# Kernel optimization log

Hardware: AMD Instinct MI355X
Metric: run time of the kernel (lower is better)

## Reference

```python
import jax, jax.numpy as jnp
import numpy as np
import math

HIDDEN = 1024
HEADS = 16
HEAD_DIM = HIDDEN // HEADS
TEMP_K = 1000.0  # custom temperature multiplier applied after masking
B, S = 2, 2048


def setup_inputs() -> dict:
    key = jax.random.key(0)
    ks = jax.random.split(key, 4)
    scale = 1.0 / math.sqrt(HIDDEN)
    return {
        "x": jax.random.normal(ks[0], (B, S, HIDDEN), dtype=jnp.float32),
        "W_qkv": jax.random.normal(ks[1], (HIDDEN, 3 * HIDDEN), dtype=jnp.float32) * scale,
        "b_qkv": jnp.zeros((3 * HIDDEN,), dtype=jnp.float32),
        "W_out": jax.random.normal(ks[2], (HIDDEN, HIDDEN), dtype=jnp.float32) * scale,
        "b_out": jnp.zeros((HIDDEN,), dtype=jnp.float32),
    }


def reference(x, W_qkv, b_qkv, W_out, b_out):
    b, s, _ = x.shape
    qkv = x @ W_qkv + b_qkv                                    # [b,s,3*hidden]
    qkv = qkv.reshape(b, s, 3, HEADS, HEAD_DIM)
    qkv = jnp.transpose(qkv, (2, 0, 3, 1, 4))                  # [3,b,h,s,d]
    q, k, v = qkv[0], qkv[1], qkv[2]
    scores = jnp.einsum('bhqd,bhkd->bhqk', q, k) / math.sqrt(HEAD_DIM)
    causal = jnp.tril(jnp.ones((s, s), dtype=bool))            # [s,s]
    scores = jnp.where(causal[None, None], scores, -jnp.inf)
    probs = jax.nn.softmax(scores * TEMP_K, axis=-1)           # temp-scaled softmax
    attn = jnp.einsum('bhqk,bhkd->bhqd', probs, v)             # [b,h,s,d]
    attn = jnp.transpose(attn, (0, 2, 1, 3)).reshape(b, s, HIDDEN)
    return attn @ W_out + b_out
```

## Files before the change

### kernel.cpp

```cpp
#include <hip/hip_runtime.h>
#include <hip/hip_bf16.h>

#define BATCH 2
#define SEQ 2048
#define HID 1024
#define NHEAD 16
#define HDIM 64
#define LSCALE 125.0f
#define NEGBIG (-1.0e30f)

typedef __bf16 bf16;
typedef __bf16 bf16x4 __attribute__((ext_vector_type(4)));
typedef __bf16 bf16x8 __attribute__((ext_vector_type(8)));
typedef float f32x16 __attribute__((ext_vector_type(16)));

__global__ __launch_bounds__(256) void transpose_split_kernel(
    const float* __restrict__ W, bf16* __restrict__ Thi, bf16* __restrict__ Tlo,
    int K, int N)
{
    __shared__ float T[64][65];
    const int tid = threadIdx.x;
    const int kBase = blockIdx.y * 64;
    const int nBase = blockIdx.x * 64;
    {
        const int k0 = tid >> 4;
        const int nc = (tid & 15) * 4;
#pragma unroll
        for (int kk = 0; kk < 4; kk++) {
            int k = k0 + kk * 16;
            float4 v = *(const float4*)(W + (size_t)(kBase + k) * N + nBase + nc);
            T[k][nc] = v.x; T[k][nc + 1] = v.y; T[k][nc + 2] = v.z; T[k][nc + 3] = v.w;
        }
    }
    __syncthreads();
    {
        const int n = tid >> 2;
        const int kc = (tid & 3) * 16;
        bf16x8 h0, h1, l0, l1;
#pragma unroll
        for (int j = 0; j < 8; j++) {
            float a = T[kc + j][n];
            float c = T[kc + 8 + j][n];
            bf16 ha = (bf16)a, hc = (bf16)c;
            h0[j] = ha; h1[j] = hc;
            l0[j] = (bf16)(a - (float)ha);
            l1[j] = (bf16)(c - (float)hc);
        }
        size_t dst = (size_t)(nBase + n) * K + kBase + kc;
        *(bf16x8*)(Thi + dst)     = h0;
        *(bf16x8*)(Thi + dst + 8) = h1;
        if (Tlo) {
            *(bf16x8*)(Tlo + dst)     = l0;
            *(bf16x8*)(Tlo + dst + 8) = l1;
        }
    }
}

__global__ __launch_bounds__(256) void gemm_qkv_mfma(
    const float* __restrict__ X, const bf16* __restrict__ Wthi,
    const bf16* __restrict__ Wtlo, const float* __restrict__ bias,
    bf16* __restrict__ qhi, bf16* __restrict__ qlo,
    bf16* __restrict__ khi, bf16* __restrict__ klo, bf16* __restrict__ vv)
{
    __shared__ __align__(16) bf16 Xh[128][40];
    __shared__ __align__(16) bf16 Xl[128][40];
    __shared__ __align__(16) bf16 Wh[128][40];
    __shared__ __align__(16) bf16 Wl[128][40];

    const int tid = threadIdx.x;
    const int wave = tid >> 6, lane = tid & 63;
    const int lm = lane & 31, lq2 = lane >> 5;
    const int wave_s = wave & 1, wave_n = wave >> 1;
    const int nBase = blockIdx.x * 128;
    const int sBase = blockIdx.y * 128;
    const bool isV = (nBase >= 2 * HID);

    const int sr = tid >> 1, skc = (tid & 1) * 16;

    f32x16 acc[2][2];
#pragma unroll
    for (int st = 0; st < 2; st++)
#pragma unroll
      for (int nt = 0; nt < 2; nt++)
#pragma unroll
        for (int r = 0; r < 16; r++) acc[st][nt][r] = 0.f;

    for (int k0 = 0; k0 < HID; k0 += 32) {
        const float4* px = (const float4*)(X + (size_t)(sBase + sr) * HID + k0 + skc);
        float4 x0 = px[0], x1 = px[1], x2 = px[2], x3 = px[3];
        size_t wsrc = (size_t)(nBase + sr) * HID + k0 + skc;
        bf16x8 wh0 = *(const bf16x8*)(Wthi + wsrc);
        bf16x8 wh1 = *(const bf16x8*)(Wthi + wsrc + 8);
        bf16x8 wl0 = {}, wl1 = {};
        if (!isV) {
            wl0 = *(const bf16x8*)(Wtlo + wsrc);
            wl1 = *(const bf16x8*)(Wtlo + wsrc + 8);
        }
        __syncthreads();
        {
            float xs[16] = {x0.x, x0.y, x0.z, x0.w, x1.x, x1.y, x1.z, x1.w,
                            x2.x, x2.y, x2.z, x2.w, x3.x, x3.y, x3.z, x3.w};
            bf16x8 hh0, hh1;
#pragma unroll
            for (int j = 0; j < 8; j++) { hh0[j] = (bf16)xs[j]; hh1[j] = (bf16)xs[j + 8]; }
            *(bf16x8*)&Xh[sr][skc]     = hh0;
            *(bf16x8*)&Xh[sr][skc + 8] = hh1;
            if (!isV) {
                bf16x8 ll0, ll1;
#pragma unroll
                for (int j = 0; j < 8; j++) {
                    ll0[j] = (bf16)(xs[j] - (float)hh0[j]);
                    ll1[j] = (bf16)(xs[j + 8] - (float)hh1[j]);
                }
                *(bf16x8*)&Xl[sr][skc]     = ll0;
                *(bf16x8*)&Xl[sr][skc + 8] = ll1;
            }
        }
        *(bf16x8*)&Wh[sr][skc]     = wh0;
        *(bf16x8*)&Wh[sr][skc + 8] = wh1;
        if (!isV) {
            *(bf16x8*)&Wl[sr][skc]     = wl0;
            *(bf16x8*)&Wl[sr][skc + 8] = wl1;
        }
        __syncthreads();

#pragma unroll
        for (int kh = 0; kh < 2; kh++) {
            const int ko = kh * 16 + lq2 * 8;
            bf16x8 aWh[2], aWl[2], bXh[2], bXl[2];
#pragma unroll
            for (int nt = 0; nt < 2; nt++) {
                aWh[nt] = *(bf16x8*)&Wh[wave_n * 64 + nt * 32 + lm][ko];
                if (!isV) aWl[nt] = *(bf16x8*)&Wl[wave_n * 64 + nt * 32 + lm][ko];
            }
#pragma unroll
            for (int st = 0; st < 2; st++) {
                bXh[st] = *(bf16x8*)&Xh[wave_s * 64 + st * 32 + lm][ko];
                if (!isV) bXl[st] = *(bf16x8*)&Xl[wave_s * 64 + st * 32 + lm][ko];
            }
#pragma unroll
            for (int nt = 0; nt < 2; nt++)
#pragma unroll
              for (int st = 0; st < 2; st++) {
                acc[st][nt] = __builtin_amdgcn_mfma_f32_32x32x16_bf16(aWh[nt], bXh[st], acc[st][nt], 0, 0, 0);
                if (!isV) {
                    acc[st][nt] = __builtin_amdgcn_mfma_f32_32x32x16_bf16(aWh[nt], bXl[st], acc[st][nt], 0, 0, 0);
                    acc[st][nt] = __builtin_amdgcn_mfma_f32_32x32x16_bf16(aWl[nt], bXh[st], acc[st][nt], 0, 0, 0);
                }
              }
        }
    }

#pragma unroll
    for (int st = 0; st < 2; st++) {
        int s = sBase + wave_s * 64 + st * 32 + lm;
        int bb = s >> 11, ss = s & 2047;
#pragma unroll
        for (int nt = 0; nt < 2; nt++) {
#pragma unroll
            for (int q4 = 0; q4 < 4; q4++) {
                int n = nBase + wave_n * 64 + nt * 32 + 8 * q4 + 4 * lq2;
                float4 bv = *(const float4*)(bias + n);
                float vals[4];
                vals[0] = acc[st][nt][q4 * 4 + 0] + bv.x;
                vals[1] = acc[st][nt][q4 * 4 + 1] + bv.y;
                vals[2] = acc[st][nt][q4 * 4 + 2] + bv.z;
                vals[3] = acc[st][nt][q4 * 4 + 3] + bv.w;
                int which = n >> 10, h = (n >> 6) & 15, d = n & 63;
                size_t dst = (((size_t)bb * NHEAD + h) * SEQ + ss) * HDIM + d;
                if (which < 2) {
                    bf16x4 hi4, lo4;
#pragma unroll
                    for (int i = 0; i < 4; i++) {
                        hi4[i] = (bf16)vals[i];
                        lo4[i] = (bf16)(vals[i] - (float)hi4[i]);
                    }
                    bf16* ph = (which == 0) ? qhi : khi;
                    bf16* pl = (which == 0) ? qlo : klo;
                    *(bf16x4*)(ph + dst) = hi4;
                    *(bf16x4*)(pl + dst) = lo4;
                } else {
                    bf16x4 v4;
#pragma unroll
                    for (int i = 0; i < 4; i++) v4[i] = (bf16)vals[i];
                    *(bf16x4*)(vv + dst) = v4;
                }
            }
        }
    }
}

__global__ __launch_bounds__(256) void attn_kernel(
    const bf16* __restrict__ Qhi, const bf16* __restrict__ Qlo,
    const bf16* __restrict__ Khg, const bf16* __restrict__ Klg,
    const bf16* __restrict__ Vg, bf16* __restrict__ attnbuf)
{
    __shared__ __align__(16) bf16 Khs[64][72];
    __shared__ __align__(16) bf16 Kls[64][72];
    __shared__ __align__(16) bf16 Vt [64][72];
    __shared__ __align__(16) bf16 Pb [128][72];

    const int tid  = threadIdx.x;
    const int wave = tid >> 6;
    const int lane = tid & 63;
    const int lm   = lane & 31;
    const int lq2  = lane >> 5;

    const int qt = 15 - blockIdx.x;
    const int bh = blockIdx.y;
    const int b = bh >> 4, h = bh & 15;
    const size_t headoff = ((size_t)b * NHEAD + h) * SEQ * HDIM;

    const int qg = qt * 128 + wave * 32 + lm;
    bf16x8 qh[4], ql[4];
    {
        const bf16* qph = Qhi + headoff + (size_t)qg * HDIM;
        const bf16* qpl = Qlo + headoff + (size_t)qg * HDIM;
#pragma unroll
        for (int c = 0; c < 4; c++) {
            qh[c] = *(const bf16x8*)(qph + c * 16 + lq2 * 8);
            ql[c] = *(const bf16x8*)(qpl + c * 16 + lq2 * 8);
        }
    }

    const int kr  = tid >> 2;
    const int kd0 = (tid & 3) * 16;
    const int vd  = tid & 63;
    const int vc0 = (tid >> 6) * 16;

    f32x16 O0, O1;
#pragma unroll
    for (int r = 0; r < 16; r++) { O0[r] = 0.f; O1[r] = 0.f; }
    float m_run = NEGBIG, l_run = 0.f;

    const int ktmax = 2 * qt + 1;
    for (int kt = 0; kt <= ktmax; kt++) {
        size_t kbase_g = headoff + (size_t)(kt * 64 + kr) * HDIM + kd0;
        bf16x8 kh0 = *(const bf16x8*)(Khg + kbase_g);
        bf16x8 kh1 = *(const bf16x8*)(Khg + kbase_g + 8);
        bf16x8 kl0 = *(const bf16x8*)(Klg + kbase_g);
        bf16x8 kl1 = *(const bf16x8*)(Klg + kbase_g + 8);
        bf16 vtmp[16];
#pragma unroll
        for (int i = 0; i < 16; i++)
            vtmp[i] = Vg[headoff + (size_t)(kt * 64 + vc0 + i) * HDIM + vd];

        __syncthreads();

        *(bf16x8*)&Khs[kr][kd0]     = kh0;
        *(bf16x8*)&Khs[kr][kd0 + 8] = kh1;
        *(bf16x8*)&Kls[kr][kd0]     = kl0;
        *(bf16x8*)&Kls[kr][kd0 + 8] = kl1;
        {
            bf16x8 v0, v1;
#pragma unroll
            for (int i = 0; i < 8; i++) { v0[i] = vtmp[i]; v1[i] = vtmp[i + 8]; }
            *(bf16x8*)&Vt[vd][vc0]     = v0;
            *(bf16x8*)&Vt[vd][vc0 + 8] = v1;
        }
        __syncthreads();

        f32x16 s0, s1;
#pragma unroll
        for (int r = 0; r < 16; r++) { s0[r] = 0.f; s1[r] = 0.f; }
#pragma unroll
        for (int c = 0; c < 4; c++) {
            bf16x8 ah0 = *(bf16x8*)&Khs[lm][c * 16 + lq2 * 8];
            bf16x8 al0 = *(bf16x8*)&Kls[lm][c * 16 + lq2 * 8];
            bf16x8 ah1 = *(bf16x8*)&Khs[32 + lm][c * 16 + lq2 * 8];
            bf16x8 al1 = *(bf16x8*)&Kls[32 + lm][c * 16 + lq2 * 8];
            s0 = __builtin_amdgcn_mfma_f32_32x32x16_bf16(ah0, qh[c], s0, 0, 0, 0);
            s0 = __builtin_amdgcn_mfma_f32_32x32x16_bf16(ah0, ql[c], s0, 0, 0, 0);
            s0 = __builtin_amdgcn_mfma_f32_32x32x16_bf16(al0, qh[c], s0, 0, 0, 0);
            s1 = __builtin_amdgcn_mfma_f32_32x32x16_bf16(ah1, qh[c], s1, 0, 0, 0);
            s1 = __builtin_amdgcn_mfma_f32_32x32x16_bf16(ah1, ql[c], s1, 0, 0, 0);
            s1 = __builtin_amdgcn_mfma_f32_32x32x16_bf16(al1, qh[c], s1, 0, 0, 0);
        }

        float logit[2][16];
        const int kbase = kt * 64 + 4 * lq2;
        const bool needmask = (kt * 64 + 63 > qg);
#pragma unroll
        for (int r = 0; r < 16; r++) {
            int koff = (r & 3) + 8 * (r >> 2);
            float L0 = s0[r] * LSCALE;
            float L1 = s1[r] * LSCALE;
            if (needmask) {
                if (kbase + koff > qg) L0 = NEGBIG;
                if (kbase + 32 + koff > qg) L1 = NEGBIG;
            }
            logit[0][r] = L0;
            logit[1][r] = L1;
        }

        float vmax = NEGBIG;
#pragma unroll
        for (int r = 0; r < 16; r++)
            vmax = fmaxf(vmax, fmaxf(logit[0][r], logit[1][r]));
        vmax = fmaxf(vmax, __shfl_xor(vmax, 32, 64));
        float mnew = fmaxf(m_run, vmax);
        float alpha = __expf(m_run - mnew);
        float p[2][16];
        float sum = 0.f;
#pragma unroll
        for (int r = 0; r < 16; r++) {
            p[0][r] = __expf(logit[0][r] - mnew);
            p[1][r] = __expf(logit[1][r] - mnew);
            sum += p[0][r] + p[1][r];
        }
        sum += __shfl_xor(sum, 32, 64);
        l_run = l_run * alpha + sum;
        m_run = mnew;
#pragma unroll
        for (int r = 0; r < 16; r++) { O0[r] *= alpha; O1[r] *= alpha; }

#pragma unroll
        for (int mt = 0; mt < 2; mt++)
#pragma unroll
          for (int g = 0; g < 4; g++) {
            bf16x4 pk;
            pk[0] = (bf16)p[mt][4 * g + 0];
            pk[1] = (bf16)p[mt][4 * g + 1];
            pk[2] = (bf16)p[mt][4 * g + 2];
            pk[3] = (bf16)p[mt][4 * g + 3];
            *(bf16x4*)&Pb[wave * 32 + lm][mt * 32 + 8 * g + 4 * lq2] = pk;
          }
        asm volatile("s_waitcnt lgkmcnt(0)" ::: "memory");

#pragma unroll
        for (int c = 0; c < 4; c++) {
            bf16x8 pb  = *(bf16x8*)&Pb[wave * 32 + lm][c * 16 + lq2 * 8];
            bf16x8 va0 = *(bf16x8*)&Vt[lm][c * 16 + lq2 * 8];
            bf16x8 va1 = *(bf16x8*)&Vt[32 + lm][c * 16 + lq2 * 8];
            O0 = __builtin_amdgcn_mfma_f32_32x32x16_bf16(va0, pb, O0, 0, 0, 0);
            O1 = __builtin_amdgcn_mfma_f32_32x32x16_bf16(va1, pb, O1, 0, 0, 0);
        }
    }

    const float inv = 1.0f / l_run;
    bf16* orow = attnbuf + ((size_t)b * SEQ + qg) * HID + h * HDIM;
#pragma unroll
    for (int g = 0; g < 4; g++) {
        int d0 = 8 * g + 4 * lq2;
        bf16x4 o0, o1;
#pragma unroll
        for (int i = 0; i < 4; i++) {
            o0[i] = (bf16)(O0[4 * g + i] * inv);
            o1[i] = (bf16)(O1[4 * g + i] * inv);
        }
        *(bf16x4*)(orow + d0)      = o0;
        *(bf16x4*)(orow + 32 + d0) = o1;
    }
}

__global__ __launch_bounds__(256) void gemm_out_mfma(
    const bf16* __restrict__ Attn, const bf16* __restrict__ Wt,
    const float* __restrict__ bias, float* __restrict__ out)
{
    __shared__ __align__(16) bf16 Ah[128][40];
    __shared__ __align__(16) bf16 Bh[128][40];

    const int tid = threadIdx.x;
    const int wave = tid >> 6, lane = tid & 63;
    const int lm = lane & 31, lq2 = lane >> 5;
    const int wave_m = wave & 1, wave_n = wave >> 1;
    const int nBase = blockIdx.x * 128;
    const int mBase = blockIdx.y * 128;

    const int sr = tid >> 1, skc = (tid & 1) * 16;

    f32x16 acc[2][2];
#pragma unroll
    for (int mt = 0; mt < 2; mt++)
#pragma unroll
      for (int nt = 0; nt < 2; nt++)
#pragma unroll
        for (int r = 0; r < 16; r++) acc[mt][nt][r] = 0.f;

    for (int k0 = 0; k0 < HID; k0 += 32) {
        size_t asrc = (size_t)(nBase + sr) * HID + k0 + skc;
        size_t bsrc = (size_t)(mBase + sr) * HID + k0 + skc;
        bf16x8 a0 = *(const bf16x8*)(Wt + asrc);
        bf16x8 a1 = *(const bf16x8*)(Wt + asrc + 8);
        bf16x8 b0 = *(const bf16x8*)(Attn + bsrc);
        bf16x8 b1 = *(const bf16x8*)(Attn + bsrc + 8);
        __syncthreads();
        *(bf16x8*)&Ah[sr][skc]     = a0;
        *(bf16x8*)&Ah[sr][skc + 8] = a1;
        *(bf16x8*)&Bh[sr][skc]     = b0;
        *(bf16x8*)&Bh[sr][skc + 8] = b1;
        __syncthreads();
#pragma unroll
        for (int kh = 0; kh < 2; kh++) {
            const int ko = kh * 16 + lq2 * 8;
            bf16x8 aW[2], bA[2];
#pragma unroll
            for (int nt = 0; nt < 2; nt++)
                aW[nt] = *(bf16x8*)&Ah[wave_n * 64 + nt * 32 + lm][ko];
#pragma unroll
            for (int mt = 0; mt < 2; mt++)
                bA[mt] = *(bf16x8*)&Bh[wave_m * 64 + mt * 32 + lm][ko];
#pragma unroll
            for (int nt = 0; nt < 2; nt++)
#pragma unroll
              for (int mt = 0; mt < 2; mt++)
                acc[mt][nt] = __builtin_amdgcn_mfma_f32_32x32x16_bf16(aW[nt], bA[mt], acc[mt][nt], 0, 0, 0);
        }
    }

#pragma unroll
    for (int mt = 0; mt < 2; mt++) {
        int m = mBase + wave_m * 64 + mt * 32 + lm;
#pragma unroll
        for (int nt = 0; nt < 2; nt++) {
#pragma unroll
            for (int q4 = 0; q4 < 4; q4++) {
                int n = nBase + wave_n * 64 + nt * 32 + 8 * q4 + 4 * lq2;
                float4 bv = *(const float4*)(bias + n);
                float4 o;
                o.x = acc[mt][nt][q4 * 4 + 0] + bv.x;
                o.y = acc[mt][nt][q4 * 4 + 1] + bv.y;
                o.z = acc[mt][nt][q4 * 4 + 2] + bv.z;
                o.w = acc[mt][nt][q4 * 4 + 3] + bv.w;
                *(float4*)(out + (size_t)m * HID + n) = o;
            }
        }
    }
}

extern "C" void kernel_launch(void* const* d_in, const int* in_sizes, int n_in,
                              void* d_out, int out_size, void* d_ws, size_t ws_size,
                              hipStream_t stream) {
    const float* x    = (const float*)d_in[0];
    const float* Wqkv = (const float*)d_in[1];
    const float* bqkv = (const float*)d_in[2];
    const float* Wout = (const float*)d_in[3];
    const float* bout = (const float*)d_in[4];
    float* out = (float*)d_out;

    const size_t NW  = (size_t)HID * 3 * HID;
    const size_t NWo = (size_t)HID * HID;
    const size_t NT  = (size_t)BATCH * NHEAD * SEQ * HDIM;
    bf16* Wthi = (bf16*)d_ws;
    bf16* Wtlo = Wthi + NW;
    bf16* Wot  = Wtlo + NW;
    bf16* qhi  = Wot + NWo;
    bf16* qlo  = qhi + NT;
    bf16* khi  = qlo + NT;
    bf16* klo  = khi + NT;
    bf16* vv   = klo + NT;
    bf16* attnbuf = vv + NT;

    transpose_split_kernel<<<dim3(3 * HID / 64, HID / 64), 256, 0, stream>>>(
        Wqkv, Wthi, Wtlo, HID, 3 * HID);
    transpose_split_kernel<<<dim3(HID / 64, HID / 64), 256, 0, stream>>>(
        Wout, Wot, nullptr, HID, HID);
    gemm_qkv_mfma<<<dim3(3 * HID / 128, BATCH * SEQ / 128), 256, 0, stream>>>(
        x, Wthi, Wtlo, bqkv, qhi, qlo, khi, klo, vv);
    attn_kernel<<<dim3(SEQ / 128, BATCH * NHEAD), 256, 0, stream>>>(
        qhi, qlo, khi, klo, vv, attnbuf);
    gemm_out_mfma<<<dim3(HID / 128, BATCH * SEQ / 128), 256, 0, stream>>>(
        attnbuf, Wot, bout, out);
}
```

Measured before the change: 289.2 us.

## Pre-split X, add atomic work queue to attention, shrink output GEMM tile

A new kernel converts X into bf16 hi/lo halves once, so the QKV GEMM stops redoing that conversion in every N-block and reads half as many bytes per element. The attention kernel becomes persistent: 768 blocks pull (query-tile, head) items from an atomic counter, heaviest causal tiles first, to balance the uneven causal work across CUs. The output GEMM uses 128x64 tiles instead of 128x128, doubling the block count to fill the GPU better. The costs are an extra launch plus hi/lo X buffers that reuse the attention output workspace, atomic contention on one counter, and less data reuse per block in the output GEMM.

After: 298.7 us. 1.03x slower.

```diff
diff --git a/kernel.cpp b/kernel.cpp
--- a/kernel.cpp
+++ b/kernel.cpp
@@ -8,6 +8,7 @@
 #define HDIM 64
 #define LSCALE 125.0f
 #define NEGBIG (-1.0e30f)
+#define N_ITEMS 512
 
 typedef __bf16 bf16;
 typedef __bf16 bf16x4 __attribute__((ext_vector_type(4)));
@@ -56,9 +57,28 @@
     }
 }
 
+__global__ __launch_bounds__(256) void xsplit_kernel(
+    const float* __restrict__ X, bf16* __restrict__ Xhi, bf16* __restrict__ Xlo,
+    unsigned* __restrict__ ctr)
+{
+    if (blockIdx.x == 0 && threadIdx.x == 0) *ctr = 0u;
+    const int i = blockIdx.x * 256 + threadIdx.x;
+    float4 v = ((const float4*)X)[i];
+    float xs[4] = {v.x, v.y, v.z, v.w};
+    bf16x4 h, l;
+#pragma unroll
+    for (int j = 0; j < 4; j++) {
+        h[j] = (bf16)xs[j];
+        l[j] = (bf16)(xs[j] - (float)h[j]);
+    }
+    ((bf16x4*)Xhi)[i] = h;
+    ((bf16x4*)Xlo)[i] = l;
+}
+
 __global__ __launch_bounds__(256) void gemm_qkv_mfma(
-    const float* __restrict__ X, const bf16* __restrict__ Wthi,
-    const bf16* __restrict__ Wtlo, const float* __restrict__ bias,
+    const bf16* __restrict__ Xhi, const bf16* __restrict__ Xlo,
+    const bf16* __restrict__ Wthi, const bf16* __restrict__ Wtlo,
+    const float* __restrict__ bias,
     bf16* __restrict__ qhi, bf16* __restrict__ qlo,
     bf16* __restrict__ khi, bf16* __restrict__ klo, bf16* __restrict__ vv)
 {
@@ -86,39 +106,27 @@
         for (int r = 0; r < 16; r++) acc[st][nt][r] = 0.f;
 
     for (int k0 = 0; k0 < HID; k0 += 32) {
-        const float4* px = (const float4*)(X + (size_t)(sBase + sr) * HID + k0 + skc);
-        float4 x0 = px[0], x1 = px[1], x2 = px[2], x3 = px[3];
+        size_t xsrc = (size_t)(sBase + sr) * HID + k0 + skc;
         size_t wsrc = (size_t)(nBase + sr) * HID + k0 + skc;
+        bf16x8 xh0 = *(const bf16x8*)(Xhi + xsrc);
+        bf16x8 xh1 = *(const bf16x8*)(Xhi + xsrc + 8);
         bf16x8 wh0 = *(const bf16x8*)(Wthi + wsrc);
         bf16x8 wh1 = *(const bf16x8*)(Wthi + wsrc + 8);
-        bf16x8 wl0 = {}, wl1 = {};
+        bf16x8 xl0 = {}, xl1 = {}, wl0 = {}, wl1 = {};
         if (!isV) {
+            xl0 = *(const bf16x8*)(Xlo + xsrc);
+            xl1 = *(const bf16x8*)(Xlo + xsrc + 8);
             wl0 = *(const bf16x8*)(Wtlo + wsrc);
             wl1 = *(const bf16x8*)(Wtlo + wsrc + 8);
         }
         __syncthreads();
-        {
-            float xs[16] = {x0.x, x0.y, x0.z, x0.w, x1.x, x1.y, x1.z, x1.w,
-                            x2.x, x2.y, x2.z, x2.w, x3.x, x3.y, x3.z, x3.w};
-            bf16x8 hh0, hh1;
-#pragma unroll
-            for (int j = 0; j < 8; j++) { hh0[j] = (bf16)xs[j]; hh1[j] = (bf16)xs[j + 8]; }
-            *(bf16x8*)&Xh[sr][skc]     = hh0;
-            *(bf16x8*)&Xh[sr][skc + 8] = hh1;
-            if (!isV) {
-                bf16x8 ll0, ll1;
-#pragma unroll
-                for (int j = 0; j < 8; j++) {
-                    ll0[j] = (bf16)(xs[j] - (float)hh0[j]);
-                    ll1[j] = (bf16)(xs[j + 8] - (float)hh1[j]);
-                }
-                *(bf16x8*)&Xl[sr][skc]     = ll0;
-                *(bf16x8*)&Xl[sr][skc + 8] = ll1;
-            }
-        }
+        *(bf16x8*)&Xh[sr][skc]     = xh0;
+        *(bf16x8*)&Xh[sr][skc + 8] = xh1;
         *(bf16x8*)&Wh[sr][skc]     = wh0;
         *(bf16x8*)&Wh[sr][skc + 8] = wh1;
         if (!isV) {
+            *(bf16x8*)&Xl[sr][skc]     = xl0;
+            *(bf16x8*)&Xl[sr][skc + 8] = xl1;
             *(bf16x8*)&Wl[sr][skc]     = wl0;
             *(bf16x8*)&Wl[sr][skc + 8] = wl1;
         }
@@ -193,12 +201,14 @@
 __global__ __launch_bounds__(256) void attn_kernel(
     const bf16* __restrict__ Qhi, const bf16* __restrict__ Qlo,
     const bf16* __restrict__ Khg, const bf16* __restrict__ Klg,
-    const bf16* __restrict__ Vg, bf16* __restrict__ attnbuf)
+    const bf16* __restrict__ Vg, bf16* __restrict__ attnbuf,
+    unsigned* __restrict__ ctr)
 {
     __shared__ __align__(16) bf16 Khs[64][72];
     __shared__ __align__(16) bf16 Kls[64][72];
     __shared__ __align__(16) bf16 Vt [64][72];
     __shared__ __align__(16) bf16 Pb [128][72];
+    __shared__ int s_item;
 
     const int tid  = threadIdx.x;
     const int wave = tid >> 6;
@@ -206,150 +216,156 @@
     const int lm   = lane & 31;
     const int lq2  = lane >> 5;
 
-    const int qt = 15 - blockIdx.x;
-    const int bh = blockIdx.y;
-    const int b = bh >> 4, h = bh & 15;
-    const size_t headoff = ((size_t)b * NHEAD + h) * SEQ * HDIM;
-
-    const int qg = qt * 128 + wave * 32 + lm;
-    bf16x8 qh[4], ql[4];
-    {
-        const bf16* qph = Qhi + headoff + (size_t)qg * HDIM;
-        const bf16* qpl = Qlo + headoff + (size_t)qg * HDIM;
-#pragma unroll
-        for (int c = 0; c < 4; c++) {
-            qh[c] = *(const bf16x8*)(qph + c * 16 + lq2 * 8);
-            ql[c] = *(const bf16x8*)(qpl + c * 16 + lq2 * 8);
-        }
-    }
-
     const int kr  = tid >> 2;
     const int kd0 = (tid & 3) * 16;
     const int vd  = tid & 63;
     const int vc0 = (tid >> 6) * 16;
 
-    f32x16 O0, O1;
-#pragma unroll
-    for (int r = 0; r < 16; r++) { O0[r] = 0.f; O1[r] = 0.f; }
-    float m_run = NEGBIG, l_run = 0.f;
-
-    const int ktmax = 2 * qt + 1;
-    for (int kt = 0; kt <= ktmax; kt++) {
-        size_t kbase_g = headoff + (size_t)(kt * 64 + kr) * HDIM + kd0;
-        bf16x8 kh0 = *(const bf16x8*)(Khg + kbase_g);
-        bf16x8 kh1 = *(const bf16x8*)(Khg + kbase_g + 8);
-        bf16x8 kl0 = *(const bf16x8*)(Klg + kbase_g);
-        bf16x8 kl1 = *(const bf16x8*)(Klg + kbase_g + 8);
-        bf16 vtmp[16];
-#pragma unroll
-        for (int i = 0; i < 16; i++)
-            vtmp[i] = Vg[headoff + (size_t)(kt * 64 + vc0 + i) * HDIM + vd];
-
+    for (;;) {
+        if (tid == 0) s_item = (int)atomicAdd(ctr, 1u);
         __syncthreads();
-
-        *(bf16x8*)&Khs[kr][kd0]     = kh0;
-        *(bf16x8*)&Khs[kr][kd0 + 8] = kh1;
-        *(bf16x8*)&Kls[kr][kd0]     = kl0;
-        *(bf16x8*)&Kls[kr][kd0 + 8] = kl1;
+        const int it = s_item;
+        if (it >= N_ITEMS) return;
+        const int qt = 15 - (it >> 5);
+        const int bh = it & 31;
+        const int b = bh >> 4, h = bh & 15;
+        const size_t headoff = ((size_t)b * NHEAD + h) * SEQ * HDIM;
+
+        const int qg = qt * 128 + wave * 32 + lm;
+        bf16x8 qh[4], ql[4];
         {
-            bf16x8 v0, v1;
-#pragma unroll
-            for (int i = 0; i < 8; i++) { v0[i] = vtmp[i]; v1[i] = vtmp[i + 8]; }
-            *(bf16x8*)&Vt[vd][vc0]     = v0;
-            *(bf16x8*)&Vt[vd][vc0 + 8] = v1;
-        }
-        __syncthreads();
-
-        f32x16 s0, s1;
-#pragma unroll
-        for (int r = 0; r < 16; r++) { s0[r] = 0.f; s1[r] = 0.f; }
-#pragma unroll
-        for (int c = 0; c < 4; c++) {
-            bf16x8 ah0 = *(bf16x8*)&Khs[lm][c * 16 + lq2 * 8];
-            bf16x8 al0 = *(bf16x8*)&Kls[lm][c * 16 + lq2 * 8];
-            bf16x8 ah1 = *(bf16x8*)&Khs[32 + lm][c * 16 + lq2 * 8];
-            bf16x8 al1 = *(bf16x8*)&Kls[32 + lm][c * 16 + lq2 * 8];
-            s0 = __builtin_amdgcn_mfma_f32_32x32x16_bf16(ah0, qh[c], s0, 0, 0, 0);
-            s0 = __builtin_amdgcn_mfma_f32_32x32x16_bf16(ah0, ql[c], s0, 0, 0, 0);
-            s0 = __builtin_amdgcn_mfma_f32_32x32x16_bf16(al0, qh[c], s0, 0, 0, 0);
-            s1 = __builtin_amdgcn_mfma_f32_32x32x16_bf16(ah1, qh[c], s1, 0, 0, 0);
-            s1 = __builtin_amdgcn_mfma_f32_32x32x16_bf16(ah1, ql[c], s1, 0, 0, 0);
-            s1 = __builtin_amdgcn_mfma_f32_32x32x16_bf16(al1, qh[c], s1, 0, 0, 0);
-        }
-
-        float logit[2][16];
-        const int kbase = kt * 64 + 4 * lq2;
-        const bool needmask = (kt * 64 + 63 > qg);
-#pragma unroll
-        for (int r = 0; r < 16; r++) {
-            int koff = (r & 3) + 8 * (r >> 2);
-            float L0 = s0[r] * LSCALE;
-            float L1 = s1[r] * LSCALE;
-            if (needmask) {
-                if (kbase + koff > qg) L0 = NEGBIG;
-                if (kbase + 32 + koff > qg) L1 = NEGBIG;
-            }
-            logit[0][r] = L0;
-            logit[1][r] = L1;
-        }
-
-        float vmax = NEGBIG;
-#pragma unroll
-        for (int r = 0; r < 16; r++)
-            vmax = fmaxf(vmax, fmaxf(logit[0][r], logit[1][r]));
-        vmax = fmaxf(vmax, __shfl_xor(vmax, 32, 64));
-        float mnew = fmaxf(m_run, vmax);
-        float alpha = __expf(m_run - mnew);
-        float p[2][16];
-        float sum = 0.f;
-#pragma unroll
-        for (int r = 0; r < 16; r++) {
-            p[0][r] = __expf(logit[0][r] - mnew);
-            p[1][r] = __expf(logit[1][r] - mnew);
-            sum += p[0][r] + p[1][r];
-        }
-        sum += __shfl_xor(sum, 32, 64);
-        l_run = l_run * alpha + sum;
-        m_run = mnew;
-#pragma unroll
-        for (int r = 0; r < 16; r++) { O0[r] *= alpha; O1[r] *= alpha; }
-
-#pragma unroll
-        for (int mt = 0; mt < 2; mt++)
-#pragma unroll
-          for (int g = 0; g < 4; g++) {
-            bf16x4 pk;
-            pk[0] = (bf16)p[mt][4 * g + 0];
-            pk[1] = (bf16)p[mt][4 * g + 1];
-            pk[2] = (bf16)p[mt][4 * g + 2];
-            pk[3] = (bf16)p[mt][4 * g + 3];
-            *(bf16x4*)&Pb[wave * 32 + lm][mt * 32 + 8 * g + 4 * lq2] = pk;
-          }
-        asm volatile("s_waitcnt lgkmcnt(0)" ::: "memory");
-
-#pragma unroll
-        for (int c = 0; c < 4; c++) {
-            bf16x8 pb  = *(bf16x8*)&Pb[wave * 32 + lm][c * 16 + lq2 * 8];
-            bf16x8 va0 = *(bf16x8*)&Vt[lm][c * 16 + lq2 * 8];
-            bf16x8 va1 = *(bf16x8*)&Vt[32 + lm][c * 16 + lq2 * 8];
-            O0 = __builtin_amdgcn_mfma_f32_32x32x16_bf16(va0, pb, O0, 0, 0, 0);
-            O1 = __builtin_amdgcn_mfma_f32_32x32x16_bf16(va1, pb, O1, 0, 0, 0);
-        }
-    }
-
-    const float inv = 1.0f / l_run;
-    bf16* orow = attnbuf + ((size_t)b * SEQ + qg) * HID + h * HDIM;
-#pragma unroll
-    for (int g = 0; g < 4; g++) {
-        int d0 = 8 * g + 4 * lq2;
-        bf16x4 o0, o1;
-#pragma unroll
-        for (int i = 0; i < 4; i++) {
-            o0[i] = (bf16)(O0[4 * g + i] * inv);
-            o1[i] = (bf16)(O1[4 * g + i] * inv);
-        }
-        *(bf16x4*)(orow + d0)      = o0;
-        *(bf16x4*)(orow + 32 + d0) = o1;
+            const bf16* qph = Qhi + headoff + (size_t)qg * HDIM;
+            const bf16* qpl = Qlo + headoff + (size_t)qg * HDIM;
+#pragma unroll
+            for (int c = 0; c < 4; c++) {
+                qh[c] = *(const bf16x8*)(qph + c * 16 + lq2 * 8);
+                ql[c] = *(const bf16x8*)(qpl + c * 16 + lq2 * 8);
+            }
+        }
+
+        f32x16 O0, O1;
+#pragma unroll
+        for (int r = 0; r < 16; r++) { O0[r] = 0.f; O1[r] = 0.f; }
+        float m_run = NEGBIG, l_run = 0.f;
+
+        const int ktmax = 2 * qt + 1;
+        for (int kt = 0; kt <= ktmax; kt++) {
+            size_t kbase_g = headoff + (size_t)(kt * 64 + kr) * HDIM + kd0;
+            bf16x8 kh0 = *(const bf16x8*)(Khg + kbase_g);
+            bf16x8 kh1 = *(const bf16x8*)(Khg + kbase_g + 8);
+            bf16x8 kl0 = *(const bf16x8*)(Klg + kbase_g);
+            bf16x8 kl1 = *(const bf16x8*)(Klg + kbase_g + 8);
+            bf16 vtmp[16];
+#pragma unroll
+            for (int i = 0; i < 16; i++)
+                vtmp[i] = Vg[headoff + (size_t)(kt * 64 + vc0 + i) * HDIM + vd];
+
+            __syncthreads();
+
+            *(bf16x8*)&Khs[kr][kd0]     = kh0;
+            *(bf16x8*)&Khs[kr][kd0 + 8] = kh1;
+            *(bf16x8*)&Kls[kr][kd0]     = kl0;
+            *(bf16x8*)&Kls[kr][kd0 + 8] = kl1;
+            {
+                bf16x8 v0, v1;
+#pragma unroll
+                for (int i = 0; i < 8; i++) { v0[i] = vtmp[i]; v1[i] = vtmp[i + 8]; }
+                *(bf16x8*)&Vt[vd][vc0]     = v0;
+                *(bf16x8*)&Vt[vd][vc0 + 8] = v1;
+            }
+            __syncthreads();
+
+            f32x16 s0, s1;
+#pragma unroll
+            for (int r = 0; r < 16; r++) { s0[r] = 0.f; s1[r] = 0.f; }
+#pragma unroll
+            for (int c = 0; c < 4; c++) {
+                bf16x8 ah0 = *(bf16x8*)&Khs[lm][c * 16 + lq2 * 8];
+                bf16x8 al0 = *(bf16x8*)&Kls[lm][c * 16 + lq2 * 8];
+                bf16x8 ah1 = *(bf16x8*)&Khs[32 + lm][c * 16 + lq2 * 8];
+                bf16x8 al1 = *(bf16x8*)&Kls[32 + lm][c * 16 + lq2 * 8];
+                s0 = __builtin_amdgcn_mfma_f32_32x32x16_bf16(ah0, qh[c], s0, 0, 0, 0);
+                s0 = __builtin_amdgcn_mfma_f32_32x32x16_bf16(ah0, ql[c], s0, 0, 0, 0);
+                s0 = __builtin_amdgcn_mfma_f32_32x32x16_bf16(al0, qh[c], s0, 0, 0, 0);
+                s1 = __builtin_amdgcn_mfma_f32_32x32x16_bf16(ah1, qh[c], s1, 0, 0, 0);
+                s1 = __builtin_amdgcn_mfma_f32_32x32x16_bf16(ah1, ql[c], s1, 0, 0, 0);
+                s1 = __builtin_amdgcn_mfma_f32_32x32x16_bf16(al1, qh[c], s1, 0, 0, 0);
+            }
+
+            float logit[2][16];
+            const int kbase = kt * 64 + 4 * lq2;
+            const bool needmask = (kt * 64 + 63 > qg);
+#pragma unroll
+            for (int r = 0; r < 16; r++) {
+                int koff = (r & 3) + 8 * (r >> 2);
+                float L0 = s0[r] * LSCALE;
+                float L1 = s1[r] * LSCALE;
+                if (needmask) {
+                    if (kbase + koff > qg) L0 = NEGBIG;
+                    if (kbase + 32 + koff > qg) L1 = NEGBIG;
+                }
+                logit[0][r] = L0;
+                logit[1][r] = L1;
+            }
+
+            float vmax = NEGBIG;
+#pragma unroll
+            for (int r = 0; r < 16; r++)
+                vmax = fmaxf(vmax, fmaxf(logit[0][r], logit[1][r]));
+            vmax = fmaxf(vmax, __shfl_xor(vmax, 32, 64));
+            float mnew = fmaxf(m_run, vmax);
+            float alpha = __expf(m_run - mnew);
+            float p[2][16];
+            float sum = 0.f;
+#pragma unroll
+            for (int r = 0; r < 16; r++) {
+                p[0][r] = __expf(logit[0][r] - mnew);
+                p[1][r] = __expf(logit[1][r] - mnew);
+                sum += p[0][r] + p[1][r];
+            }
+            sum += __shfl_xor(sum, 32, 64);
+            l_run = l_run * alpha + sum;
+            m_run = mnew;
+#pragma unroll
+            for (int r = 0; r < 16; r++) { O0[r] *= alpha; O1[r] *= alpha; }
+
+#pragma unroll
+            for (int mt = 0; mt < 2; mt++)
+#pragma unroll
+              for (int g = 0; g < 4; g++) {
+                bf16x4 pk;
+                pk[0] = (bf16)p[mt][4 * g + 0];
+                pk[1] = (bf16)p[mt][4 * g + 1];
+                pk[2] = (bf16)p[mt][4 * g + 2];
+                pk[3] = (bf16)p[mt][4 * g + 3];
+                *(bf16x4*)&Pb[wave * 32 + lm][mt * 32 + 8 * g + 4 * lq2] = pk;
+              }
+            asm volatile("s_waitcnt lgkmcnt(0)" ::: "memory");
+
+#pragma unroll
+            for (int c = 0; c < 4; c++) {
+                bf16x8 pb  = *(bf16x8*)&Pb[wave * 32 + lm][c * 16 + lq2 * 8];
+                bf16x8 va0 = *(bf16x8*)&Vt[lm][c * 16 + lq2 * 8];
+                bf16x8 va1 = *(bf16x8*)&Vt[32 + lm][c * 16 + lq2 * 8];
+                O0 = __builtin_amdgcn_mfma_f32_32x32x16_bf16(va0, pb, O0, 0, 0, 0);
+                O1 = __builtin_amdgcn_mfma_f32_32x32x16_bf16(va1, pb, O1, 0, 0, 0);
+            }
+        }
+
+        const float inv = 1.0f / l_run;
+        bf16* orow = attnbuf + ((size_t)b * SEQ + qg) * HID + h * HDIM;
+#pragma unroll
+        for (int g = 0; g < 4; g++) {
+            int d0 = 8 * g + 4 * lq2;
+            bf16x4 o0, o1;
+#pragma unroll
+            for (int i = 0; i < 4; i++) {
+                o0[i] = (bf16)(O0[4 * g + i] * inv);
+                o1[i] = (bf16)(O1[4 * g + i] * inv);
+            }
+            *(bf16x4*)(orow + d0)      = o0;
+            *(bf16x4*)(orow + 32 + d0) = o1;
+        }
     }
 }
 
@@ -357,73 +373,59 @@
     const bf16* __restrict__ Attn, const bf16* __restrict__ Wt,
     const float* __restrict__ bias, float* __restrict__ out)
 {
-    __shared__ __align__(16) bf16 Ah[128][40];
+    __shared__ __align__(16) bf16 Ah[64][40];
     __shared__ __align__(16) bf16 Bh[128][40];
 
     const int tid = threadIdx.x;
     const int wave = tid >> 6, lane = tid & 63;
     const int lm = lane & 31, lq2 = lane >> 5;
-    const int wave_m = wave & 1, wave_n = wave >> 1;
-    const int nBase = blockIdx.x * 128;
+    const int nBase = blockIdx.x * 64;
     const int mBase = blockIdx.y * 128;
 
     const int sr = tid >> 1, skc = (tid & 1) * 16;
-
-    f32x16 acc[2][2];
-#pragma unroll
-    for (int mt = 0; mt < 2; mt++)
-#pragma unroll
-      for (int nt = 0; nt < 2; nt++)
-#pragma unroll
-        for (int r = 0; r < 16; r++) acc[mt][nt][r] = 0.f;
+    const int ar = tid >> 2, akc = (tid & 3) * 8;
+
+    f32x16 acc[2];
+#pragma unroll
+    for (int nt = 0; nt < 2; nt++)
+#pragma unroll
+      for (int r = 0; r < 16; r++) acc[nt][r] = 0.f;
 
     for (int k0 = 0; k0 < HID; k0 += 32) {
-        size_t asrc = (size_t)(nBase + sr) * HID + k0 + skc;
         size_t bsrc = (size_t)(mBase + sr) * HID + k0 + skc;
-        bf16x8 a0 = *(const bf16x8*)(Wt + asrc);
-        bf16x8 a1 = *(const bf16x8*)(Wt + asrc + 8);
+        size_t asrc = (size_t)(nBase + ar) * HID + k0 + akc;
         bf16x8 b0 = *(const bf16x8*)(Attn + bsrc);
         bf16x8 b1 = *(const bf16x8*)(Attn + bsrc + 8);
+        bf16x8 a0 = *(const bf16x8*)(Wt + asrc);
         __syncthreads();
-        *(bf16x8*)&Ah[sr][skc]     = a0;
-        *(bf16x8*)&Ah[sr][skc + 8] = a1;
         *(bf16x8*)&Bh[sr][skc]     = b0;
         *(bf16x8*)&Bh[sr][skc + 8] = b1;
+        *(bf16x8*)&Ah[ar][akc]     = a0;
         __syncthreads();
 #pragma unroll
         for (int kh = 0; kh < 2; kh++) {
             const int ko = kh * 16 + lq2 * 8;
-            bf16x8 aW[2], bA[2];
-#pragma unroll
-            for (int nt = 0; nt < 2; nt++)
-                aW[nt] = *(bf16x8*)&Ah[wave_n * 64 + nt * 32 + lm][ko];
-#pragma unroll
-            for (int mt = 0; mt < 2; mt++)
-                bA[mt] = *(bf16x8*)&Bh[wave_m * 64 + mt * 32 + lm][ko];
-#pragma unroll
-            for (int nt = 0; nt < 2; nt++)
-#pragma unroll
-              for (int mt = 0; mt < 2; mt++)
-                acc[mt][nt] = __builtin_amdgcn_mfma_f32_32x32x16_bf16(aW[nt], bA[mt], acc[mt][nt], 0, 0, 0);
-        }
-    }
-
-#pragma unroll
-    for (int mt = 0; mt < 2; mt++) {
-        int m = mBase + wave_m * 64 + mt * 32 + lm;
-#pragma unroll
-        for (int nt = 0; nt < 2; nt++) {
-#pragma unroll
-            for (int q4 = 0; q4 < 4; q4++) {
-                int n = nBase + wave_n * 64 + nt * 32 + 8 * q4 + 4 * lq2;
-                float4 bv = *(const float4*)(bias + n);
-                float4 o;
-                o.x = acc[mt][nt][q4 * 4 + 0] + bv.x;
-                o.y = acc[mt][nt][q4 * 4 + 1] + bv.y;
-                o.z = acc[mt][nt][q4 * 4 + 2] + bv.z;
-                o.w = acc[mt][nt][q4 * 4 + 3] + bv.w;
-                *(float4*)(out + (size_t)m * HID + n) = o;
-            }
+            bf16x8 bA  = *(bf16x8*)&Bh[wave * 32 + lm][ko];
+            bf16x8 aW0 = *(bf16x8*)&Ah[lm][ko];
+            bf16x8 aW1 = *(bf16x8*)&Ah[32 + lm][ko];
+            acc[0] = __builtin_amdgcn_mfma_f32_32x32x16_bf16(aW0, bA, acc[0], 0, 0, 0);
+            acc[1] = __builtin_amdgcn_mfma_f32_32x32x16_bf16(aW1, bA, acc[1], 0, 0, 0);
+        }
+    }
+
+    const int m = mBase + wave * 32 + lm;
+#pragma unroll
+    for (int nt = 0; nt < 2; nt++) {
+#pragma unroll
+        for (int q4 = 0; q4 < 4; q4++) {
+            int n = nBase + nt * 32 + 8 * q4 + 4 * lq2;
+            float4 bv = *(const float4*)(bias + n);
+            float4 o;
+            o.x = acc[nt][q4 * 4 + 0] + bv.x;
+            o.y = acc[nt][q4 * 4 + 1] + bv.y;
+            o.z = acc[nt][q4 * 4 + 2] + bv.z;
+            o.w = acc[nt][q4 * 4 + 3] + bv.w;
+            *(float4*)(out + (size_t)m * HID + n) = o;
         }
     }
 }
@@ -450,15 +452,19 @@
     bf16* klo  = khi + NT;
     bf16* vv   = klo + NT;
     bf16* attnbuf = vv + NT;
-
+    bf16* Xhi  = attnbuf;
+    bf16* Xlo  = attnbuf + NT;
+    unsigned* ctr = (unsigned*)(Xlo + NT);
+
+    xsplit_kernel<<<dim3((BATCH * SEQ * HID) / 1024), 256, 0, stream>>>(x, Xhi, Xlo, ctr);
     transpose_split_kernel<<<dim3(3 * HID / 64, HID / 64), 256, 0, stream>>>(
         Wqkv, Wthi, Wtlo, HID, 3 * HID);
     transpose_split_kernel<<<dim3(HID / 64, HID / 64), 256, 0, stream>>>(
         Wout, Wot, nullptr, HID, HID);
     gemm_qkv_mfma<<<dim3(3 * HID / 128, BATCH * SEQ / 128), 256, 0, stream>>>(
-        x, Wthi, Wtlo, bqkv, qhi, qlo, khi, klo, vv);
-    attn_kernel<<<dim3(SEQ / 128, BATCH * NHEAD), 256, 0, stream>>>(
-        qhi, qlo, khi, klo, vv, attnbuf);
-    gemm_out_mfma<<<dim3(HID / 128, BATCH * SEQ / 128), 256, 0, stream>>>(
+        Xhi, Xlo, Wthi, Wtlo, bqkv, qhi, qlo, khi, klo, vv);
+    attn_kernel<<<dim3(768), 256, 0, stream>>>(
+        qhi, qlo, khi, klo, vv, attnbuf, ctr);
+    gemm_out_mfma<<<dim3(HID / 64, BATCH * SEQ / 128), 256, 0, stream>>>(
         attnbuf, Wot, bout, out);
 }
```
